# Kernel optimization log

Measured on AMD Instinct MI355X. Metric: run time of the kernel, lower is better.

The kernel has to match this reference:

```python
import jax, jax.numpy as jnp
import numpy as np
from jax import lax
from jax.scipy.special import erf

EPS = 1e-5
B = 256

def _conv(x, w, stride):
    return lax.conv_general_dilated(x, w, (stride, stride), ((1, 1), (1, 1)),
                                    dimension_numbers=('NCHW', 'OIHW', 'NCHW'))

def lr_conv(x, alpha, betta, bias, stride):
    # Ternary weight distribution (LR-nets): p0 = P(w=0), p1 = P(w=1)
    p0 = jax.nn.sigmoid(alpha)
    p1 = (1.0 - p0) * jax.nn.sigmoid(betta)
    w_mean = 2.0 * p1 + p0 - 1.0          # E[w] = p1 - p_{-1}
    w_var = (1.0 - p0) - w_mean * w_mean  # Var[w] = E[w^2] - E[w]^2
    m = _conv(x, w_mean, stride) + bias[None, :, None, None]
    v = _conv(x * x, w_var, stride)
    return m, v

def sign_prob(m, v):
    # expected sign under CLT Gaussian: 2*Phi(m/sqrt(v)) - 1 = erf(m / sqrt(2 v))
    return erf(m / jnp.sqrt(2.0 * (v + EPS)))

def setup_inputs() -> dict:
    key = jax.random.key(0)
    ks = jax.random.split(key, 32)
    def n(k, shape, s=1.0):
        return jax.random.normal(k, shape, dtype=jnp.float32) * s
    inp = {}
    inp['x'] = n(ks[0], (B, 3, 32, 32))
    shapes = [(128, 3), (128, 128), (256, 128), (256, 256), (512, 256), (512, 512)]
    i = 1
    for li, (co, ci) in enumerate(shapes, start=1):
        inp['a%d' % li] = n(ks[i], (co, ci, 3, 3)); i += 1
        inp['b%d' % li] = n(ks[i], (co, ci, 3, 3)); i += 1
        inp['c%d' % li] = jnp.zeros((co,), jnp.float32)
    inp['bn_gamma'] = jnp.ones((512,), jnp.float32)
    inp['bn_beta'] = jnp.zeros((512,), jnp.float32)
    inp['fc1_w'] = n(ks[20], (1024, 8192), 0.01)
    inp['fc1_b'] = jnp.zeros((1024,), jnp.float32)
    inp['fc2_w'] = n(ks[21], (10, 1024), 0.03)
    inp['fc2_b'] = jnp.zeros((10,), jnp.float32)
    inp['noise6'] = n(ks[22], (B, 512, 4, 4))
    return inp

def reference(x, a1, b1, c1, a2, b2, c2, a3, b3, c3, a4, b4, c4, a5, b5, c5,
              a6, b6, c6, bn_gamma, bn_beta, fc1_w, fc1_b, fc2_w, fc2_b, noise6):
    h = x
    for (a, bt, c, s) in [(a1, b1, c1, 1), (a2, b2, c2, 2), (a3, b3, c3, 1),
                          (a4, b4, c4, 2), (a5, b5, c5, 1)]:
        m, v = lr_conv(h, a, bt, c, s)
        h = sign_prob(m, v)
    m, v = lr_conv(h, a6, b6, c6, 2)          # output_sample=True layer
    z = m + jnp.sqrt(v + EPS) * noise6        # reparameterized Gaussian sample
    mu = jnp.mean(z, axis=(0, 2, 3), keepdims=True)
    var = jnp.var(z, axis=(0, 2, 3), keepdims=True)
    z = bn_gamma[None, :, None, None] * (z - mu) / jnp.sqrt(var + EPS) + bn_beta[None, :, None, None]
    z = jax.nn.relu(z).reshape(z.shape[0], -1)  # [B, 8192]
    z = jax.nn.relu(z @ fc1_w.T + fc1_b)
    return z @ fc2_w.T + fc2_b
```

## Files before the change

kernel.cpp:

```cpp
#include <hip/hip_runtime.h>
#include <hip/hip_bf16.h>
#include <math.h>

#define EPS 1e-5f

typedef __hip_bfloat16 bf16;
typedef short s16x8 __attribute__((ext_vector_type(8)));
typedef float f32x4 __attribute__((ext_vector_type(4)));

constexpr int ilog2c(int v) { return v <= 1 ? 0 : 1 + ilog2c(v >> 1); }

__device__ __forceinline__ float ldin(const void* p, size_t i, int isbf) {
    return isbf ? __bfloat162float(((const bf16*)p)[i]) : ((const float*)p)[i];
}
__device__ __forceinline__ float b2f_bits(short s) {
    unsigned u = ((unsigned)(unsigned short)s) << 16;
    return __builtin_bit_cast(float, u);
}
__device__ __forceinline__ unsigned sqpk1(unsigned w) {
    float lo = __builtin_bit_cast(float, w << 16);
    float hi = __builtin_bit_cast(float, w & 0xffff0000u);
    lo *= lo; hi *= hi;
    unsigned ul = __builtin_bit_cast(unsigned, lo) + 0x8000u;
    unsigned uh = __builtin_bit_cast(unsigned, hi) + 0x8000u;
    return __builtin_amdgcn_perm(uh, ul, 0x07060302);
}
__device__ __forceinline__ uint4 sqpk4(uint4 u) {
    uint4 r;
    r.x = sqpk1(u.x); r.y = sqpk1(u.y); r.z = sqpk1(u.z); r.w = sqpk1(u.w);
    return r;
}

__device__ __forceinline__ void dma16(const void* g, void* l) {
    __builtin_amdgcn_global_load_lds(
        (const __attribute__((address_space(1))) void*)g,
        (__attribute__((address_space(3))) void*)l, 16, 0, 0);
}

__global__ __launch_bounds__(64) void detect_kernel(const void* __restrict__ x,
                                                    int* __restrict__ flags,
                                                    char* __restrict__ gA,
                                                    char* __restrict__ gB) {
    const unsigned* w = (const unsigned*)x;
    unsigned word = w[threadIdx.x];
    int e = (word >> 23) & 0xFF;
    bool ok = (word == 0u) || (e >= 0x70 && e <= 0x8E);
    unsigned long long m = __ballot(ok);
    if (threadIdx.x == 0) flags[0] = (__popcll(m) >= 32) ? 0 : 1;
    uint4 z4 = (uint4){0, 0, 0, 0};
#pragma unroll
    for (int k = 0; k < 2; k++) {
        ((uint4*)gA)[threadIdx.x * 2 + k] = z4;
        ((uint4*)gB)[threadIdx.x * 2 + k] = z4;
    }
}

__global__ __launch_bounds__(256) void prep_w_l1(
    const void* __restrict__ alpha, const void* __restrict__ betta,
    const int* __restrict__ flags, float* __restrict__ wmv, int n)
{
    int i = blockIdx.x * 256 + threadIdx.x;
    if (i >= n) return;
    int fl = flags[0];
    float a = ldin(alpha, i, fl), b = ldin(betta, i, fl);
    float p0 = 1.f / (1.f + expf(-a));
    float p1 = (1.f - p0) / (1.f + expf(-b));
    float m = 2.f * p1 + p0 - 1.f;
    wmv[i] = m;
    wmv[n + i] = (1.f - p0) - m * m;
}

__global__ __launch_bounds__(256) void prep_w_r(
    const void* __restrict__ alpha, const void* __restrict__ betta,
    const int* __restrict__ flags, bf16* __restrict__ wmr, bf16* __restrict__ wvr,
    int lc, int n)
{
    int o = blockIdx.x * 256 + threadIdx.x;
    if (o >= n) return;
    int fl = flags[0];
    int cotap = o >> lc;
    int ci = o & ((1 << lc) - 1);
    int co = cotap / 9;
    int tap = cotap - co * 9;
    int i = (((co << lc) + ci) * 9) + tap;
    float a = ldin(alpha, i, fl), b = ldin(betta, i, fl);
    float p0 = 1.f / (1.f + expf(-a));
    float p1 = (1.f - p0) / (1.f + expf(-b));
    float m = 2.f * p1 + p0 - 1.f;
    float v = (1.f - p0) - m * m;
    wmr[o] = __float2bfloat16(m);
    wvr[o] = __float2bfloat16(v);
}

__global__ __launch_bounds__(256) void permute_fc1(
    const void* __restrict__ w, const int* __restrict__ flags, bf16* __restrict__ wp)
{
    __shared__ float L[8192];
    const int fl = flags[0];
    int tid = threadIdx.x;
    int o = blockIdx.x;
    size_t srow = (size_t)o * 8192;
    for (int c = tid; c < 512; c += 256) {
        float v[16];
        if (fl) {
            const uint4* s = (const uint4*)((const bf16*)w + srow + c * 16);
            uint4 u0 = s[0], u1 = s[1];
            const unsigned short* h0 = (const unsigned short*)&u0;
            const unsigned short* h1 = (const unsigned short*)&u1;
#pragma unroll
            for (int j = 0; j < 8; j++) { v[j] = b2f_bits((short)h0[j]); v[8 + j] = b2f_bits((short)h1[j]); }
        } else {
            const float4* s = (const float4*)((const float*)w + srow + c * 16);
#pragma unroll
            for (int j = 0; j < 4; j++) {
                float4 t4 = s[j];
                v[j * 4 + 0] = t4.x; v[j * 4 + 1] = t4.y; v[j * 4 + 2] = t4.z; v[j * 4 + 3] = t4.w;
            }
        }
#pragma unroll
        for (int hw = 0; hw < 16; hw++) L[hw * 512 + c] = v[hw];
    }
    __syncthreads();
    for (int j = 0; j < 32; j++) {
        int idx = j * 256 + tid;
        wp[srow + idx] = __float2bfloat16(L[idx]);
    }
}

__global__ __launch_bounds__(256) void l1_conv(
    const void* __restrict__ x, const float* __restrict__ wmv,
    const void* __restrict__ bias, const int* __restrict__ flags,
    bf16* __restrict__ out)
{
    __shared__ float Xs[64][28];
    const int fl = flags[0];
    int tid = threadIdx.x;
    int pos0 = blockIdx.x * 64;
    int b = pos0 >> 10;
    for (int u = tid; u < 576; u += 256) {
        int p = u / 9, r = u - p * 9;
        int ci = r / 3, kh = r - ci * 3;
        int pos = pos0 + p;
        int oh = (pos >> 5) & 31, ow = pos & 31;
        int ih = oh - 1 + kh;
        bool okh = (unsigned)ih < 32u;
        size_t base = ((size_t)(b * 3 + ci) * 32 + ih) * 32;
#pragma unroll
        for (int kw = 0; kw < 3; kw++) {
            int iw = ow - 1 + kw;
            float v = (okh && (unsigned)iw < 32u) ? ldin(x, base + iw, fl) : 0.f;
            Xs[p][ci * 9 + kh * 3 + kw] = v;
        }
    }
    int c = tid & 127, pg = tid >> 7;
    float wm[27], wv[27];
#pragma unroll
    for (int k = 0; k < 27; k++) {
        wm[k] = wmv[c * 27 + k];
        wv[k] = wmv[3456 + c * 27 + k];
    }
    float bs = ldin(bias, c, fl);
    __syncthreads();
    for (int it = 0; it < 32; it++) {
        int p = it * 2 + pg;
        float aM = 0.f, aV = 0.f;
#pragma unroll
        for (int k = 0; k < 27; k++) {
            float xv = Xs[p][k];
            aM = fmaf(xv, wm[k], aM);
            aV = fmaf(xv * xv, wv[k], aV);
        }
        out[(size_t)(pos0 + p) * 128 + c] =
            __float2bfloat16(erff((aM + bs) * rsqrtf(2.f * (aV + EPS))));
    }
}

template<int CI, int CO, int H, int W, int S, int OH, int OW, int ACT, int COT>
__global__ __launch_bounds__(256, 3) void conv_gemm(
    const char* __restrict__ xreg,
    int zpoff,
    const bf16* __restrict__ wmr,
    const bf16* __restrict__ wvr,
    const void* __restrict__ bias, const void* __restrict__ noise,
    const int* __restrict__ flags, void* __restrict__ outp)
{
    constexpr int OHW = OH * OW;
    constexpr int KC = CI / 32;
    constexpr int LKC = ilog2c(KC);
    constexpr int NC = 9 * KC;
    constexpr int NW = COT / 16;
    constexpr int XB = 128 * 64;
    constexpr int WB = COT * 64;
    constexpr int BUFB = XB + 2 * WB;
    constexpr int LOHW = ilog2c(OHW), LOW = ilog2c(OW);
    static_assert(NC % 3 == 0 && COT == 64, "");

    __shared__ __align__(16) char smem[3 * BUFB];

    const int tid = threadIdx.x;
    const int lane = tid & 63, wv_ = tid >> 6;
    const int q = lane >> 4, l15 = lane & 15;
    const int pw = wv_ * 32;
    const int c0 = blockIdx.y * COT;
    const int bx128 = blockIdx.x * 128;

    const int sl   = (lane & 7) ^ (lane >> 3);
    const int row2 = 2 * (lane >> 3) + (sl >> 2);
    const int u16b = (sl & 3) * 16;

    int xb[4], ohS[4], owS[4];
#pragma unroll
    for (int kk = 0; kk < 4; kk++) {
        int P = bx128 + 16 * ((wv_ & 1) * 4 + kk) + row2;
        int bi = P >> LOHW;
        ohS[kk] = ((P >> LOW) & (OH - 1)) * S - 1;
        owS[kk] = (P & (OW - 1)) * S - 1;
        xb[kk] = bi * (H * W * CI * 2);
    }
    const char* wsb = (const char*)((wv_ == 3) ? wvr : wmr)
                      + (size_t)(c0 + row2) * (9 * CI * 2) + u16b;
    const int wdoff = XB + ((wv_ == 3) ? WB : 0);

    const int lA = (l15 >> 1) * 128 + (((((l15 & 1) << 2) | q) ^ (l15 >> 1)) << 4);
    const int abase = pw * 64 + lA;
    const int bbase = lA;

    f32x4 accM[2][4], accV[2][4];
#pragma unroll
    for (int i = 0; i < 2; i++)
#pragma unroll
        for (int j = 0; j < 4; j++) {
            accM[i][j] = (f32x4){0.f, 0.f, 0.f, 0.f};
            accV[i][j] = (f32x4){0.f, 0.f, 0.f, 0.f};
        }

    int curTap = -1;
    int xoffs[4];

    auto stage = [&](int t, char* buf) {
        if (wv_ < 2) {
            const int tap = t >> LKC;
            if (tap != curTap) {
                curTap = tap;
                const int kh = tap / 3, kw2 = tap - 3 * kh;
#pragma unroll
                for (int kk = 0; kk < 4; kk++) {
                    int ih = ohS[kk] + kh, iw = owS[kk] + kw2;
                    bool ok = ((unsigned)ih < (unsigned)H) && ((unsigned)iw < (unsigned)W);
                    int off = xb[kk] + (ih * W + iw) * (CI * 2) + u16b;
                    xoffs[kk] = ok ? off : zpoff;
                }
            }
            const int kci = (t & (KC - 1)) * 64;
#pragma unroll
            for (int kk = 0; kk < 4; kk++)
                dma16(xreg + xoffs[kk] + kci, buf + ((wv_ & 1) * 4 + kk) * 1024);
        } else {
            const char* s = wsb + t * 64;
            char* d = buf + wdoff;
#pragma unroll
            for (int k = 0; k < NW; k++)
                dma16(s + (size_t)k * (16 * 9 * CI * 2), d + k * 1024);
        }
    };

    auto compute = [&](const char* buf) {
        s16x8 a[2], aq[2];
#pragma unroll
        for (int i = 0; i < 2; i++) {
            a[i] = *(const s16x8*)(buf + abase + i * 1024);
            uint4 uq = sqpk4(*(const uint4*)&a[i]);
            aq[i] = *(const s16x8*)&uq;
        }
#pragma unroll
        for (int j = 0; j < 4; j++) {
            s16x8 bm = *(const s16x8*)(buf + XB + bbase + j * 1024);
            s16x8 bv = *(const s16x8*)(buf + XB + WB + bbase + j * 1024);
#pragma unroll
            for (int i = 0; i < 2; i++) {
                accM[i][j] = __builtin_amdgcn_mfma_f32_16x16x32_bf16(a[i],  bm, accM[i][j], 0, 0, 0);
                accV[i][j] = __builtin_amdgcn_mfma_f32_16x16x32_bf16(aq[i], bv, accV[i][j], 0, 0, 0);
            }
        }
    };

#define WAITBAR4() asm volatile("s_waitcnt vmcnt(4) lgkmcnt(0)\n\ts_barrier" ::: "memory")
#define WAITBAR0() asm volatile("s_waitcnt vmcnt(0) lgkmcnt(0)\n\ts_barrier" ::: "memory")

    char* const b0 = smem;
    char* const b1 = smem + BUFB;
    char* const b2 = smem + 2 * BUFB;

    stage(0, b0);
    stage(1, b1);
    for (int t = 0; t < NC; t += 3) {
        WAITBAR4();
        stage(t + 2, b2);
        compute(b0);
        WAITBAR4();
        if (t + 3 < NC) stage(t + 3, b0);
        compute(b1);
        if (t + 6 <= NC) { WAITBAR4(); } else { WAITBAR0(); }
        if (t + 4 < NC) stage(t + 4, b1);
        compute(b2);
    }
#undef WAITBAR4
#undef WAITBAR0

    __syncthreads();
    const int fl = flags[0];
    if constexpr (ACT == 0) {
        bf16* Lact = (bf16*)smem;
        constexpr int LCB = ilog2c(COT * 2);
#pragma unroll
        for (int j = 0; j < 4; j++) {
            int co = c0 + j * 16 + l15;
            float bs = ldin(bias, co, fl);
#pragma unroll
            for (int i = 0; i < 2; i++) {
#pragma unroll
                for (int r = 0; r < 4; r++) {
                    int PPl = pw + i * 16 + q * 4 + r;
                    float mm = accM[i][j][r] + bs, vv = accV[i][j][r];
                    Lact[PPl * COT + j * 16 + l15] =
                        __float2bfloat16(erff(mm * rsqrtf(2.f * (vv + EPS))));
                }
            }
        }
        __syncthreads();
        constexpr int NST = (128 * COT * 2) / 4096;
#pragma unroll
        for (int k = 0; k < NST; k++) {
            int f = k * 4096 + tid * 16;
            int rowl = f >> LCB;
            int colb = f & ((COT * 2) - 1);
            uint4 va = *(const uint4*)((char*)smem + f);
            size_t gb = ((size_t)(bx128 + rowl) * CO + c0) * 2 + colb;
            *(uint4*)((char*)outp + gb) = va;
        }
    } else {
#pragma unroll
        for (int j = 0; j < 4; j++) {
            int co = c0 + j * 16 + l15;
            float bs = ldin(bias, co, fl);
#pragma unroll
            for (int i = 0; i < 2; i++) {
#pragma unroll
                for (int r = 0; r < 4; r++) {
                    int PP = bx128 + pw + i * 16 + q * 4 + r;
                    float mm = accM[i][j][r] + bs, vv = accV[i][j][r];
                    int bb = PP / OHW, hw = PP % OHW;
                    float nz = ldin(noise, ((size_t)bb * CO + co) * OHW + hw, fl);
                    ((float*)outp)[(size_t)PP * CO + co] = mm + sqrtf(vv + EPS) * nz;
                }
            }
        }
    }
}

__global__ __launch_bounds__(256) void fc1_gemm_sk(
    const bf16* __restrict__ A, const bf16* __restrict__ Wp,
    float* __restrict__ part)
{
    __shared__ bf16 Xs[128 * 40];
    __shared__ bf16 Ws[128 * 40];
    int tid = threadIdx.x;
    int lane = tid & 63, wv_ = tid >> 6;
    int q = lane >> 4, l15 = lane & 15;
    const int pw = (wv_ >> 1) * 64, cw = (wv_ & 1) * 64;
    const int p0 = blockIdx.x * 128, c0 = blockIdx.y * 128;
    const int kb = blockIdx.z * 1024;
    const int row_i = tid >> 1, half = tid & 1;

    f32x4 acc[4][4];
#pragma unroll
    for (int i = 0; i < 4; i++)
#pragma unroll
        for (int j = 0; j < 4; j++) acc[i][j] = (f32x4){0.f, 0.f, 0.f, 0.f};

    for (int k0 = kb; k0 < kb + 1024; k0 += 32) {
        __syncthreads();
        {
            const uint4* s = (const uint4*)(A + (size_t)(p0 + row_i) * 8192 + k0 + half * 16);
            uint4* d = (uint4*)(Xs + row_i * 40 + half * 16);
            d[0] = s[0]; d[1] = s[1];
        }
        {
            const uint4* s = (const uint4*)(Wp + (size_t)(c0 + row_i) * 8192 + k0 + half * 16);
            uint4* d = (uint4*)(Ws + row_i * 40 + half * 16);
            d[0] = s[0]; d[1] = s[1];
        }
        __syncthreads();
        s16x8 a[4], bb[4];
#pragma unroll
        for (int i = 0; i < 4; i++) {
            a[i]  = *(const s16x8*)(Xs + (pw + i * 16 + l15) * 40 + q * 8);
            bb[i] = *(const s16x8*)(Ws + (cw + i * 16 + l15) * 40 + q * 8);
        }
#pragma unroll
        for (int i = 0; i < 4; i++)
#pragma unroll
            for (int j = 0; j < 4; j++)
                acc[i][j] = __builtin_amdgcn_mfma_f32_16x16x32_bf16(a[i], bb[j], acc[i][j], 0, 0, 0);
    }

    float* pbase = part + (size_t)blockIdx.z * 256 * 1024;
#pragma unroll
    for (int j = 0; j < 4; j++) {
        int co = c0 + cw + j * 16 + l15;
#pragma unroll
        for (int i = 0; i < 4; i++) {
            f32x4 m4 = acc[i][j];
#pragma unroll
            for (int r = 0; r < 4; r++) {
                int P = p0 + pw + i * 16 + q * 4 + r;
                pbase[(size_t)P * 1024 + co] = m4[r];
            }
        }
    }
}

__global__ __launch_bounds__(256) void fc1_reduce(
    const float* __restrict__ part, const void* __restrict__ bias,
    const int* __restrict__ flags, float* __restrict__ out)
{
    int i = blockIdx.x * 256 + threadIdx.x;
    float s = 0.f;
#pragma unroll
    for (int k = 0; k < 8; k++) s += part[(size_t)k * 262144 + i];
    out[i] = fmaxf(s + ldin(bias, i & 1023, flags[0]), 0.f);
}

__global__ __launch_bounds__(256) void bn_part(const float* __restrict__ z,
                                               float4* __restrict__ partial)
{
    int blk = blockIdx.x;
    int t = threadIdx.x;
    float s0 = 0, ss0 = 0, s1 = 0, ss1 = 0;
    for (int p = 0; p < 32; p++) {
        float2 v = ((const float2*)z)[((size_t)(blk * 32 + p)) * 256 + t];
        s0 += v.x; ss0 += v.x * v.x;
        s1 += v.y; ss1 += v.y * v.y;
    }
    partial[blk * 256 + t] = make_float4(s0, ss0, s1, ss1);
}

__global__ __launch_bounds__(512) void bn_fin(
    const float4* __restrict__ partial, const void* __restrict__ gamma,
    const void* __restrict__ beta, const int* __restrict__ flags,
    float* __restrict__ sc, float* __restrict__ sh)
{
    int c = threadIdx.x;
    float s = 0, ss = 0;
    for (int j = 0; j < 128; j++) {
        float4 pv = partial[j * 256 + (c >> 1)];
        s += (c & 1) ? pv.z : pv.x;
        ss += (c & 1) ? pv.w : pv.y;
    }
    float mean = s * (1.f / 4096.f);
    float var = ss * (1.f / 4096.f) - mean * mean;
    int fl = flags[0];
    float scale = ldin(gamma, c, fl) * rsqrtf(var + EPS);
    sc[c] = scale;
    sh[c] = ldin(beta, c, fl) - mean * scale;
}

__global__ __launch_bounds__(256) void bn_apply(
    const float* __restrict__ z, const float* __restrict__ sc,
    const float* __restrict__ sh, bf16* __restrict__ zr)
{
    int i = blockIdx.x * 256 + threadIdx.x;
    int c = i & 511;
    float v = z[i] * sc[c] + sh[c];
    zr[i] = __float2bfloat16(fmaxf(v, 0.f));
}

__global__ __launch_bounds__(640) void fc2_kernel(
    const float* __restrict__ A, const void* __restrict__ W,
    const void* __restrict__ bias, const int* __restrict__ flags,
    void* __restrict__ out)
{
    const int fl = flags[0];
    int n = blockIdx.x;
    int o = threadIdx.x >> 6;
    int lane = threadIdx.x & 63;
    const float* a = A + (size_t)n * 1024;
    size_t wbase = (size_t)o * 1024;
    float s = 0.f;
    for (int i = lane; i < 1024; i += 64) s = fmaf(a[i], ldin(W, wbase + i, fl), s);
#pragma unroll
    for (int off = 32; off > 0; off >>= 1) s += __shfl_down(s, off);
    if (lane == 0) {
        float v = s + ldin(bias, o, fl);
        if (fl) ((bf16*)out)[n * 10 + o] = __float2bfloat16(v);
        else    ((float*)out)[n * 10 + o] = v;
    }
}

extern "C" void kernel_launch(void* const* d_in, const int* in_sizes, int n_in,
                              void* d_out, int out_size, void* d_ws, size_t ws_size,
                              hipStream_t stream)
{
    const void* x = d_in[0];
    const void *al[6], *be[6], *bi[6];
    for (int l = 0; l < 6; l++) {
        al[l] = d_in[1 + 3 * l];
        be[l] = d_in[2 + 3 * l];
        bi[l] = d_in[3 + 3 * l];
    }
    const void* bn_gamma = d_in[19];
    const void* bn_beta  = d_in[20];
    const void* fc1_w = d_in[21];
    const void* fc1_b = d_in[22];
    const void* fc2_w = d_in[23];
    const void* fc2_b = d_in[24];
    const void* noise = d_in[25];

    char* base = (char*)d_ws;
    size_t off = 0;
    auto alloc = [&](size_t bytes) { void* p = base + off; off += (bytes + 255) & ~(size_t)255; return p; };
    int* flags = (int*)alloc(256);
    float* w1 = (float*)alloc(2 * 3456 * sizeof(float));
    const int SwLC[5] = {7, 7, 8, 8, 9};
    const size_t Sw[5] = {147456, 294912, 589824, 1179648, 2359296};
    bf16 *wmr[5], *wvr[5];
    for (int l = 0; l < 5; l++) {
        wmr[l] = (bf16*)alloc(Sw[l] * sizeof(bf16));
        wvr[l] = (bf16*)alloc(Sw[l] * sizeof(bf16));
    }
    bf16* Wp   = (bf16*)alloc((size_t)1024 * 8192 * sizeof(bf16));
    float4* part = (float4*)alloc((size_t)128 * 256 * sizeof(float4));
    float* bnsc = (float*)alloc(512 * sizeof(float));
    float* bnsh = (float*)alloc(512 * sizeof(float));
    float* fc1o = (float*)alloc((size_t)256 * 1024 * sizeof(float));
    bf16* zr   = (bf16*)alloc((size_t)256 * 8192 * sizeof(bf16));

    const int ZPA = 67108864;
    const int ZPB = 16777216;
    char* RA = (char*)alloc((size_t)ZPA + 2048);
    char* RB = (char*)alloc((size_t)ZPB + 2048);
    float* z = (float*)RB;
    float* fc1part = (float*)(RB + 8388608);

    detect_kernel<<<1, 64, 0, stream>>>(x, flags, RA + ZPA, RB + ZPB);

    prep_w_l1<<<14, 256, 0, stream>>>(al[0], be[0], flags, w1, 3456);
    for (int l = 0; l < 5; l++) {
        int n = (int)Sw[l];
        prep_w_r<<<(n + 255) / 256, 256, 0, stream>>>(
            al[l + 1], be[l + 1], flags, wmr[l], wvr[l], SwLC[l], n);
    }
    permute_fc1<<<1024, 256, 0, stream>>>(fc1_w, flags, Wp);

    l1_conv<<<4096, 256, 0, stream>>>(x, w1, bi[0], flags, (bf16*)RA);

    conv_gemm<128, 128, 32, 32, 2, 16, 16, 0, 64><<<dim3(512, 2), 256, 0, stream>>>(
        RA, ZPA, wmr[0], wvr[0], bi[1], nullptr, flags, RB);
    conv_gemm<128, 256, 16, 16, 1, 16, 16, 0, 64><<<dim3(512, 4), 256, 0, stream>>>(
        RB, ZPB, wmr[1], wvr[1], bi[2], nullptr, flags, RA);
    conv_gemm<256, 256, 16, 16, 2, 8, 8, 0, 64><<<dim3(128, 4), 256, 0, stream>>>(
        RA, ZPA, wmr[2], wvr[2], bi[3], nullptr, flags, RB);
    conv_gemm<256, 512, 8, 8, 1, 8, 8, 0, 64><<<dim3(128, 8), 256, 0, stream>>>(
        RB, ZPB, wmr[3], wvr[3], bi[4], nullptr, flags, RA);
    conv_gemm<512, 512, 8, 8, 2, 4, 4, 1, 64><<<dim3(32, 8), 256, 0, stream>>>(
        RA, ZPA, wmr[4], wvr[4], bi[5], noise, flags, z);

    bn_part<<<128, 256, 0, stream>>>(z, part);
    bn_fin<<<1, 512, 0, stream>>>(part, bn_gamma, bn_beta, flags, bnsc, bnsh);
    bn_apply<<<8192, 256, 0, stream>>>(z, bnsc, bnsh, zr);

    fc1_gemm_sk<<<dim3(2, 8, 8), 256, 0, stream>>>(zr, Wp, fc1part);
    fc1_reduce<<<1024, 256, 0, stream>>>(fc1part, fc1_b, flags, fc1o);
    fc2_kernel<<<256, 640, 0, stream>>>(fc1o, fc2_w, fc2_b, flags, d_out);
}
```

Measured before the change: 723.0 us.

## Parameterize conv_gemm position tile per wave; use 256-position tiles for layers 2-5

The conv GEMM kernel is templated on positions per wave (WPOS) and a min-waves launch bound. Layers 2-5 move from 128-position to 256-position block tiles (64 per wave), halving the grid and doubling weight reuse per staged weight tile. The cost is twice the accumulator registers and more shared memory, with occupancy dropping to 2 blocks per CU. Input offset math is now computed per tap instead of precomputed, and the wait counts are adjusted for the extra in-flight loads.

```diff
diff --git a/kernel.cpp b/kernel.cpp
--- a/kernel.cpp
+++ b/kernel.cpp
@@ -175,8 +175,8 @@
     }
 }
 
-template<int CI, int CO, int H, int W, int S, int OH, int OW, int ACT, int COT>
-__global__ __launch_bounds__(256, 3) void conv_gemm(
+template<int CI, int CO, int H, int W, int S, int OH, int OW, int ACT, int WPOS, int MINW>
+__global__ __launch_bounds__(256, MINW) void conv_gemm(
     const char* __restrict__ xreg,
     int zpoff,
     const bf16* __restrict__ wmr,
@@ -185,38 +185,31 @@
     const int* __restrict__ flags, void* __restrict__ outp)
 {
     constexpr int OHW = OH * OW;
+    constexpr int PT = WPOS * 4;
+    constexpr int MI = WPOS / 16;
     constexpr int KC = CI / 32;
     constexpr int LKC = ilog2c(KC);
     constexpr int NC = 9 * KC;
-    constexpr int NW = COT / 16;
-    constexpr int XB = 128 * 64;
-    constexpr int WB = COT * 64;
+    constexpr int NXI = PT / 32;
+    constexpr int XB = PT * 64;
+    constexpr int WB = 64 * 64;
     constexpr int BUFB = XB + 2 * WB;
     constexpr int LOHW = ilog2c(OHW), LOW = ilog2c(OW);
-    static_assert(NC % 3 == 0 && COT == 64, "");
+    static_assert(NC % 3 == 0, "");
 
     __shared__ __align__(16) char smem[3 * BUFB];
 
     const int tid = threadIdx.x;
     const int lane = tid & 63, wv_ = tid >> 6;
     const int q = lane >> 4, l15 = lane & 15;
-    const int pw = wv_ * 32;
-    const int c0 = blockIdx.y * COT;
-    const int bx128 = blockIdx.x * 128;
+    const int pw = wv_ * WPOS;
+    const int c0 = blockIdx.y * 64;
+    const int bxp = blockIdx.x * PT;
 
     const int sl   = (lane & 7) ^ (lane >> 3);
     const int row2 = 2 * (lane >> 3) + (sl >> 2);
     const int u16b = (sl & 3) * 16;
 
-    int xb[4], ohS[4], owS[4];
-#pragma unroll
-    for (int kk = 0; kk < 4; kk++) {
-        int P = bx128 + 16 * ((wv_ & 1) * 4 + kk) + row2;
-        int bi = P >> LOHW;
-        ohS[kk] = ((P >> LOW) & (OH - 1)) * S - 1;
-        owS[kk] = (P & (OW - 1)) * S - 1;
-        xb[kk] = bi * (H * W * CI * 2);
-    }
     const char* wsb = (const char*)((wv_ == 3) ? wvr : wmr)
                       + (size_t)(c0 + row2) * (9 * CI * 2) + u16b;
     const int wdoff = XB + ((wv_ == 3) ? WB : 0);
@@ -225,9 +218,9 @@
     const int abase = pw * 64 + lA;
     const int bbase = lA;
 
-    f32x4 accM[2][4], accV[2][4];
-#pragma unroll
-    for (int i = 0; i < 2; i++)
+    f32x4 accM[MI][4], accV[MI][4];
+#pragma unroll
+    for (int i = 0; i < MI; i++)
 #pragma unroll
         for (int j = 0; j < 4; j++) {
             accM[i][j] = (f32x4){0.f, 0.f, 0.f, 0.f};
@@ -235,7 +228,7 @@
         }
 
     int curTap = -1;
-    int xoffs[4];
+    int xoffs[NXI];
 
     auto stage = [&](int t, char* buf) {
         if (wv_ < 2) {
@@ -244,30 +237,33 @@
                 curTap = tap;
                 const int kh = tap / 3, kw2 = tap - 3 * kh;
 #pragma unroll
-                for (int kk = 0; kk < 4; kk++) {
-                    int ih = ohS[kk] + kh, iw = owS[kk] + kw2;
+                for (int kk = 0; kk < NXI; kk++) {
+                    int P = bxp + 16 * ((wv_ & 1) * NXI + kk) + row2;
+                    int bi = P >> LOHW;
+                    int ih = ((P >> LOW) & (OH - 1)) * S - 1 + kh;
+                    int iw = (P & (OW - 1)) * S - 1 + kw2;
                     bool ok = ((unsigned)ih < (unsigned)H) && ((unsigned)iw < (unsigned)W);
-                    int off = xb[kk] + (ih * W + iw) * (CI * 2) + u16b;
+                    int off = bi * (H * W * CI * 2) + (ih * W + iw) * (CI * 2) + u16b;
                     xoffs[kk] = ok ? off : zpoff;
                 }
             }
             const int kci = (t & (KC - 1)) * 64;
 #pragma unroll
-            for (int kk = 0; kk < 4; kk++)
-                dma16(xreg + xoffs[kk] + kci, buf + ((wv_ & 1) * 4 + kk) * 1024);
+            for (int kk = 0; kk < NXI; kk++)
+                dma16(xreg + xoffs[kk] + kci, buf + ((wv_ & 1) * NXI + kk) * 1024);
         } else {
             const char* s = wsb + t * 64;
             char* d = buf + wdoff;
 #pragma unroll
-            for (int k = 0; k < NW; k++)
+            for (int k = 0; k < 4; k++)
                 dma16(s + (size_t)k * (16 * 9 * CI * 2), d + k * 1024);
         }
     };
 
     auto compute = [&](const char* buf) {
-        s16x8 a[2], aq[2];
-#pragma unroll
-        for (int i = 0; i < 2; i++) {
+        s16x8 a[MI], aq[MI];
+#pragma unroll
+        for (int i = 0; i < MI; i++) {
             a[i] = *(const s16x8*)(buf + abase + i * 1024);
             uint4 uq = sqpk4(*(const uint4*)&a[i]);
             aq[i] = *(const s16x8*)&uq;
@@ -277,15 +273,23 @@
             s16x8 bm = *(const s16x8*)(buf + XB + bbase + j * 1024);
             s16x8 bv = *(const s16x8*)(buf + XB + WB + bbase + j * 1024);
 #pragma unroll
-            for (int i = 0; i < 2; i++) {
+            for (int i = 0; i < MI; i++) {
                 accM[i][j] = __builtin_amdgcn_mfma_f32_16x16x32_bf16(a[i],  bm, accM[i][j], 0, 0, 0);
                 accV[i][j] = __builtin_amdgcn_mfma_f32_16x16x32_bf16(aq[i], bv, accV[i][j], 0, 0, 0);
             }
         }
     };
 
-#define WAITBAR4() asm volatile("s_waitcnt vmcnt(4) lgkmcnt(0)\n\ts_barrier" ::: "memory")
-#define WAITBAR0() asm volatile("s_waitcnt vmcnt(0) lgkmcnt(0)\n\ts_barrier" ::: "memory")
+    auto waitbar = [&](bool last) {
+        if (last) {
+            asm volatile("s_waitcnt vmcnt(0) lgkmcnt(0)\n\ts_barrier" ::: "memory");
+        } else if constexpr (NXI == 8) {
+            if (wv_ < 2) asm volatile("s_waitcnt vmcnt(8) lgkmcnt(0)\n\ts_barrier" ::: "memory");
+            else         asm volatile("s_waitcnt vmcnt(4) lgkmcnt(0)\n\ts_barrier" ::: "memory");
+        } else {
+            asm volatile("s_waitcnt vmcnt(4) lgkmcnt(0)\n\ts_barrier" ::: "memory");
+        }
+    };
 
     char* const b0 = smem;
     char* const b1 = smem + BUFB;
@@ -294,48 +298,45 @@
     stage(0, b0);
     stage(1, b1);
     for (int t = 0; t < NC; t += 3) {
-        WAITBAR4();
+        waitbar(false);
         stage(t + 2, b2);
         compute(b0);
-        WAITBAR4();
+        waitbar(false);
         if (t + 3 < NC) stage(t + 3, b0);
         compute(b1);
-        if (t + 6 <= NC) { WAITBAR4(); } else { WAITBAR0(); }
+        waitbar(t + 6 > NC);
         if (t + 4 < NC) stage(t + 4, b1);
         compute(b2);
     }
-#undef WAITBAR4
-#undef WAITBAR0
 
     __syncthreads();
     const int fl = flags[0];
     if constexpr (ACT == 0) {
         bf16* Lact = (bf16*)smem;
-        constexpr int LCB = ilog2c(COT * 2);
 #pragma unroll
         for (int j = 0; j < 4; j++) {
             int co = c0 + j * 16 + l15;
             float bs = ldin(bias, co, fl);
 #pragma unroll
-            for (int i = 0; i < 2; i++) {
+            for (int i = 0; i < MI; i++) {
 #pragma unroll
                 for (int r = 0; r < 4; r++) {
                     int PPl = pw + i * 16 + q * 4 + r;
                     float mm = accM[i][j][r] + bs, vv = accV[i][j][r];
-                    Lact[PPl * COT + j * 16 + l15] =
+                    Lact[PPl * 64 + j * 16 + l15] =
                         __float2bfloat16(erff(mm * rsqrtf(2.f * (vv + EPS))));
                 }
             }
         }
         __syncthreads();
-        constexpr int NST = (128 * COT * 2) / 4096;
+        constexpr int NST = (PT * 64 * 2) / 4096;
 #pragma unroll
         for (int k = 0; k < NST; k++) {
             int f = k * 4096 + tid * 16;
-            int rowl = f >> LCB;
-            int colb = f & ((COT * 2) - 1);
+            int rowl = f >> 7;
+            int colb = f & 127;
             uint4 va = *(const uint4*)((char*)smem + f);
-            size_t gb = ((size_t)(bx128 + rowl) * CO + c0) * 2 + colb;
+            size_t gb = ((size_t)(bxp + rowl) * CO + c0) * 2 + colb;
             *(uint4*)((char*)outp + gb) = va;
         }
     } else {
@@ -344,10 +345,10 @@
             int co = c0 + j * 16 + l15;
             float bs = ldin(bias, co, fl);
 #pragma unroll
-            for (int i = 0; i < 2; i++) {
+            for (int i = 0; i < MI; i++) {
 #pragma unroll
                 for (int r = 0; r < 4; r++) {
-                    int PP = bx128 + pw + i * 16 + q * 4 + r;
+                    int PP = bxp + pw + i * 16 + q * 4 + r;
                     float mm = accM[i][j][r] + bs, vv = accV[i][j][r];
                     int bb = PP / OHW, hw = PP % OHW;
                     float nz = ldin(noise, ((size_t)bb * CO + co) * OHW + hw, fl);
@@ -554,15 +555,15 @@
 
     l1_conv<<<4096, 256, 0, stream>>>(x, w1, bi[0], flags, (bf16*)RA);
 
-    conv_gemm<128, 128, 32, 32, 2, 16, 16, 0, 64><<<dim3(512, 2), 256, 0, stream>>>(
+    conv_gemm<128, 128, 32, 32, 2, 16, 16, 0, 64, 2><<<dim3(256, 2), 256, 0, stream>>>(
         RA, ZPA, wmr[0], wvr[0], bi[1], nullptr, flags, RB);
-    conv_gemm<128, 256, 16, 16, 1, 16, 16, 0, 64><<<dim3(512, 4), 256, 0, stream>>>(
+    conv_gemm<128, 256, 16, 16, 1, 16, 16, 0, 64, 2><<<dim3(256, 4), 256, 0, stream>>>(
         RB, ZPB, wmr[1], wvr[1], bi[2], nullptr, flags, RA);
-    conv_gemm<256, 256, 16, 16, 2, 8, 8, 0, 64><<<dim3(128, 4), 256, 0, stream>>>(
+    conv_gemm<256, 256, 16, 16, 2, 8, 8, 0, 64, 2><<<dim3(64, 4), 256, 0, stream>>>(
         RA, ZPA, wmr[2], wvr[2], bi[3], nullptr, flags, RB);
-    conv_gemm<256, 512, 8, 8, 1, 8, 8, 0, 64><<<dim3(128, 8), 256, 0, stream>>>(
+    conv_gemm<256, 512, 8, 8, 1, 8, 8, 0, 64, 2><<<dim3(64, 8), 256, 0, stream>>>(
         RB, ZPB, wmr[3], wvr[3], bi[4], nullptr, flags, RA);
-    conv_gemm<512, 512, 8, 8, 2, 4, 4, 1, 64><<<dim3(32, 8), 256, 0, stream>>>(
+    conv_gemm<512, 512, 8, 8, 2, 4, 4, 1, 32, 3><<<dim3(32, 8), 256, 0, stream>>>(
         RA, ZPA, wmr[4], wvr[4], bi[5], noise, flags, z);
 
     bn_part<<<128, 256, 0, stream>>>(z, part);
```

Result: slower. 855.9 us (+18.4%).
